# Kernel optimization log

Hardware: AMD Instinct MI355X
Metric: run time of the kernel (lower is better)

Reference implementation:

```python
import jax, jax.numpy as jnp
import numpy as np

EPS = 1e-5  # torch BatchNorm2d default eps


def _conv(x, w, pad=0, groups=1):
    # x: NCHW, w: OIHW (torch layout); matches nn.Conv2d with given padding/groups
    return jax.lax.conv_general_dilated(
        x, w, window_strides=(1, 1), padding=[(pad, pad), (pad, pad)],
        dimension_numbers=("NCHW", "OIHW", "NCHW"), feature_group_count=groups)


def _bn_train(x, gamma, beta):
    # BatchNorm2d in training mode: batch stats over (N,H,W), biased variance
    m = jnp.mean(x, axis=(0, 2, 3), keepdims=True)
    v = jnp.mean(jnp.square(x - m), axis=(0, 2, 3), keepdims=True)
    return (x - m) * jax.lax.rsqrt(v + EPS) * gamma.reshape(1, -1, 1, 1) + beta.reshape(1, -1, 1, 1)


def setup_inputs() -> dict:
    key = jax.random.key(0)
    ks = jax.random.split(key, 8)
    B, C, H, W = 8, 32, 128, 128
    D = 8                      # num_directions
    WC = C * D                 # wavelet_channels = 256
    MID = WC * 2               # 512
    x = jax.random.normal(ks[0], (B, C, H, W), jnp.float32)
    # grouped directional filter bank: Conv2d(C, C*D, k=5, groups=C, bias=False)
    w_dir = jax.random.normal(ks[1], (WC, 1, 5, 5), jnp.float32) / np.sqrt(25.0)
    # wavelet_conv: Conv(WC->MID,3) BN ReLU Conv(MID->WC,3) BN ReLU
    w1 = jax.random.normal(ks[2], (MID, WC, 3, 3), jnp.float32) / np.sqrt(WC * 9.0)
    b1 = jnp.zeros((MID,), jnp.float32)
    g1 = jnp.ones((MID,), jnp.float32)
    be1 = jnp.zeros((MID,), jnp.float32)
    w2 = jax.random.normal(ks[3], (WC, MID, 3, 3), jnp.float32) / np.sqrt(MID * 9.0)
    b2 = jnp.zeros((WC,), jnp.float32)
    g2 = jnp.ones((WC,), jnp.float32)
    be2 = jnp.zeros((WC,), jnp.float32)
    # inverse_conv: Conv2d(WC, C, 1)
    w_inv = jax.random.normal(ks[4], (C, WC, 1, 1), jnp.float32) / np.sqrt(float(WC))
    b_inv = jnp.zeros((C,), jnp.float32)
    return {"x": x, "w_dir": w_dir, "w1": w1, "b1": b1, "g1": g1, "be1": be1,
            "w2": w2, "b2": b2, "g2": g2, "be2": be2, "w_inv": w_inv, "b_inv": b_inv}


def reference(x, w_dir, w1, b1, g1, be1, w2, b2, g2, be2, w_inv, b_inv):
    C = x.shape[1]
    # directional wavelet: grouped conv C -> C*8, k=5, pad=2, no bias
    coeffs = _conv(x, w_dir, pad=2, groups=C)                      # (B, 8C, H, W)
    # wavelet-domain conv stack
    h = _conv(coeffs, w1, pad=1) + b1.reshape(1, -1, 1, 1)         # (B, 16C, H, W)
    h = jax.nn.relu(_bn_train(h, g1, be1))
    h = _conv(h, w2, pad=1) + b2.reshape(1, -1, 1, 1)              # (B, 8C, H, W)
    h = jax.nn.relu(_bn_train(h, g2, be2))
    # inverse 1x1 conv back to C channels
    return _conv(h, w_inv) + b_inv.reshape(1, -1, 1, 1)            # (B, C, H, W)
```

## Files before the change

### kernel.cpp

```cpp
#include <hip/hip_runtime.h>

typedef unsigned short u16;
typedef unsigned int   u32;
typedef __attribute__((ext_vector_type(8)))  __bf16 bf16x8;
typedef __attribute__((ext_vector_type(4)))  float  f32x4;
typedef __attribute__((ext_vector_type(16))) float  f32x16;

__device__ __forceinline__ float bf2f(u16 u) {
    union { u32 i; float f; } v; v.i = ((u32)u) << 16; return v.f;
}
__device__ __forceinline__ u16 f2bf(float f) {
    u32 u = __float_as_uint(f);
    u32 r = (u + 0x7FFFu + ((u >> 16) & 1u)) >> 16;
    return (u16)r;
}

__device__ __forceinline__ void gl16(const u16* g, u16* l) {
    __builtin_amdgcn_global_load_lds(
        (const __attribute__((address_space(1))) unsigned int*)g,
        (__attribute__((address_space(3))) unsigned int*)l, 16, 0, 0);
}

__global__ __launch_bounds__(256) void dir_conv_k(const float* __restrict__ x,
                                                  const float* __restrict__ wd,
                                                  u16* __restrict__ coeffs) {
    int bid = blockIdx.x;
    int cc = bid & 3, y = (bid >> 2) & 127, n = bid >> 9;
    __shared__ float lx[5280];
    __shared__ float lw[1600];
    int t = threadIdx.x;
    for (int i = t; i < 1600; i += 256) {
        int ol = i / 25, tap = i - ol * 25;
        lw[tap * 64 + ol] = wd[(cc * 64 + ol) * 25 + tap];
    }
    for (int i = t; i < 5280; i += 256) {
        int c = i / 660, rem = i - c * 660;
        int ky = rem / 132, xx = rem - ky * 132;
        int gy = y - 2 + ky, gx = xx - 2;
        float v = 0.f;
        if (gy >= 0 && gy < 128 && gx >= 0 && gx < 128)
            v = x[(((n * 32 + cc * 8 + c) * 128 + gy) << 7) + gx];
        lx[i] = v;
    }
    __syncthreads();
    int px = t >> 1, oh = t & 1;
    float acc[4][8];
#pragma unroll
    for (int j = 0; j < 4; ++j)
#pragma unroll
        for (int d = 0; d < 8; ++d) acc[j][d] = 0.f;
#pragma unroll
    for (int j = 0; j < 4; ++j) {
        int cl = oh * 4 + j;
        const float* lxc = &lx[cl * 660];
#pragma unroll
        for (int ky = 0; ky < 5; ++ky)
#pragma unroll
            for (int kx = 0; kx < 5; ++kx) {
                float xv = lxc[ky * 132 + px + kx];
                const float* w8 = &lw[(ky * 5 + kx) * 64 + cl * 8];
#pragma unroll
                for (int d = 0; d < 8; ++d) acc[j][d] += xv * w8[d];
            }
    }
    long base = ((long)((n * 128 + y) * 128 + px)) * 256 + cc * 64 + oh * 32;
#pragma unroll
    for (int j = 0; j < 4; ++j) {
        uint4 o;
        o.x = (u32)f2bf(acc[j][0]) | ((u32)f2bf(acc[j][1]) << 16);
        o.y = (u32)f2bf(acc[j][2]) | ((u32)f2bf(acc[j][3]) << 16);
        o.z = (u32)f2bf(acc[j][4]) | ((u32)f2bf(acc[j][5]) << 16);
        o.w = (u32)f2bf(acc[j][6]) | ((u32)f2bf(acc[j][7]) << 16);
        *(uint4*)(coeffs + base + j * 8) = o;
    }
}

__global__ __launch_bounds__(256) void repack_w_k(const float* __restrict__ w,
                                                  u16* __restrict__ wp,
                                                  int OC, int IC, int total) {
    int f = blockIdx.x * 256 + threadIdx.x;
    if (f >= total) return;
    int KC = IC >> 5;
    int j  = f & 7;
    int h  = (f >> 3) & 1;
    int g  = f >> 4;
    int oc = g % OC; g /= OC;
    int s  = g & 1;  g >>= 1;
    int kc = g % KC;
    int tap = g / KC;
    int ic = kc * 32 + s * 16 + h * 8 + j;
    wp[f] = f2bf(w[(oc * IC + ic) * 9 + tap]);
}

template<int IC, int OC>
__global__ __launch_bounds__(256, 2) void conv3_k(const u16* __restrict__ base,
                                                  u32 in_off,
                                                  const u16* __restrict__ wp,
                                                  const float* __restrict__ bias,
                                                  u32 zp_off,
                                                  u16* __restrict__ outp) {
    constexpr int KC = IC / 32;
    constexpr int W  = 130;
    constexpr int TU = 12 * W;
    constexpr int NFULL = TU / 256;
    constexpr int REM   = TU % 256;
    __shared__ u16 lA0[TU * 8];
    __shared__ u16 lA1[TU * 8];

    int bx = blockIdx.x;
    int y = bx & 127, n = bx >> 7;
    int ocb = blockIdx.y;
    int t = threadIdx.x, lane = t & 63, wv = t >> 6;
    int lm = lane & 31, h = lane >> 5;
    int ocw = ocb * 256 + wv * 64;

    u32 off[NFULL + 1];
#pragma unroll
    for (int i = 0; i <= NFULL; ++i) {
        int u = (i == NFULL) ? (NFULL * 256 + lane) : (i * 256 + t);
        int icq = u / (3 * W);
        int r2  = u - icq * (3 * W);
        int dy  = r2 / W;
        int xx  = r2 - dy * W;
        int gy = y - 1 + dy, gx = xx - 1;
        bool ok = ((unsigned)gy < 128u) && ((unsigned)gx < 128u);
        off[i] = ok ? (in_off + (u32)((n * 128 + gy) * 128 + gx) * IC + (icq & 3) * 8)
                    : zp_off;
    }

    auto stage = [&](u16* dst, int kc) {
#pragma unroll
        for (int i = 0; i < NFULL; ++i)
            gl16(base + off[i] + kc * 32, dst + (i * 256 + wv * 64) * 8);
        if (wv == 0 && lane < REM)
            gl16(base + off[NFULL] + kc * 32, dst + NFULL * 256 * 8);
    };

    bf16x8 B[6][2];
    u32 wboff = (u32)(ocw + lm) * 16 + h * 8;
#pragma unroll
    for (int dx = 0; dx < 3; ++dx)
#pragma unroll
        for (int s = 0; s < 2; ++s) {
            u32 wo = wboff + (u32)((dx * KC) * 2 + s) * (OC * 16);
            B[dx * 2 + s][0] = *(const bf16x8*)(wp + wo);
            B[dx * 2 + s][1] = *(const bf16x8*)(wp + wo + 512);
        }

    f32x16 acc[4][2];
#pragma unroll
    for (int mf = 0; mf < 4; ++mf)
#pragma unroll
        for (int nf = 0; nf < 2; ++nf)
#pragma unroll
            for (int r = 0; r < 16; ++r) acc[mf][nf][r] = 0.f;

    auto compDy = [&](const u16* lAu, int dyU, int dyN, int kcN) {
#pragma unroll
        for (int dx = 0; dx < 3; ++dx)
#pragma unroll
            for (int s = 0; s < 2; ++s) {
                int i = dx * 2 + s;
                int au = (((s * 2 + h) * 3 + dyU) * W + dx + lm) * 8;
                bf16x8 a0 = *(const bf16x8*)(lAu + au);
                bf16x8 a1 = *(const bf16x8*)(lAu + au + 256);
                bf16x8 a2 = *(const bf16x8*)(lAu + au + 512);
                bf16x8 a3 = *(const bf16x8*)(lAu + au + 768);
                __builtin_amdgcn_s_setprio(1);
                acc[0][0] = __builtin_amdgcn_mfma_f32_32x32x16_bf16(a0, B[i][0], acc[0][0], 0, 0, 0);
                acc[0][1] = __builtin_amdgcn_mfma_f32_32x32x16_bf16(a0, B[i][1], acc[0][1], 0, 0, 0);
                acc[1][0] = __builtin_amdgcn_mfma_f32_32x32x16_bf16(a1, B[i][0], acc[1][0], 0, 0, 0);
                acc[1][1] = __builtin_amdgcn_mfma_f32_32x32x16_bf16(a1, B[i][1], acc[1][1], 0, 0, 0);
                acc[2][0] = __builtin_amdgcn_mfma_f32_32x32x16_bf16(a2, B[i][0], acc[2][0], 0, 0, 0);
                acc[2][1] = __builtin_amdgcn_mfma_f32_32x32x16_bf16(a2, B[i][1], acc[2][1], 0, 0, 0);
                acc[3][0] = __builtin_amdgcn_mfma_f32_32x32x16_bf16(a3, B[i][0], acc[3][0], 0, 0, 0);
                acc[3][1] = __builtin_amdgcn_mfma_f32_32x32x16_bf16(a3, B[i][1], acc[3][1], 0, 0, 0);
                __builtin_amdgcn_s_setprio(0);
                u32 wo = wboff + (u32)(((dyN * 3 + dx) * KC + kcN) * 2 + s) * (OC * 16);
                B[i][0] = *(const bf16x8*)(wp + wo);
                B[i][1] = *(const bf16x8*)(wp + wo + 512);
            }
    };

    stage(lA0, 0);
    for (int kc = 0; kc < KC; kc += 2) {
        __syncthreads();
        stage(lA1, kc + 1);
        compDy(lA0, 0, 1, kc);
        compDy(lA0, 1, 2, kc);
        compDy(lA0, 2, 0, kc + 1);
        __syncthreads();
        if (kc + 2 < KC) stage(lA0, kc + 2);
        compDy(lA1, 0, 1, kc + 1);
        compDy(lA1, 1, 2, kc + 1);
        compDy(lA1, 2, 0, (kc + 2 < KC) ? kc + 2 : 0);
    }

    long rowb = (long)(n * 128 + y) * 128;
#pragma unroll
    for (int mf = 0; mf < 4; ++mf)
#pragma unroll
        for (int nf = 0; nf < 2; ++nf) {
            int oc = ocw + nf * 32 + lm;
            float bi = bias[oc];
#pragma unroll
            for (int r = 0; r < 16; ++r) {
                int px = mf * 32 + (r & 3) + ((r >> 2) << 3) + (h << 2);
                outp[(rowb + px) * OC + oc] = f2bf(acc[mf][nf][r] + bi);
            }
        }
}

template<int C>
__global__ __launch_bounds__(256) void stats1_k(const u16* __restrict__ h,
                                                float* __restrict__ part) {
    constexpr int CH2 = C / 2;
    constexpr int PARTS = 256 / CH2;
    constexpr int RPB = 1024;
    constexpr int RPT = RPB / PARTS;
    int t = threadIdx.x;
    int chp = t % CH2, rp = t / CH2;
    long row0 = (long)blockIdx.x * RPB + (long)rp * RPT;
    float s0 = 0.f, q0 = 0.f, s1 = 0.f, q1 = 0.f;
    const u16* base = h + row0 * C + chp * 2;
    for (int r = 0; r < RPT; ++r) {
        u32 v = *(const u32*)(base + (long)r * C);
        float a = bf2f((u16)(v & 0xffff));
        float b = bf2f((u16)(v >> 16));
        s0 += a; q0 += a * a; s1 += b; q1 += b * b;
    }
    float4 o = make_float4(s0, q0, s1, q1);
    *(float4*)(part + ((long)(blockIdx.x * PARTS + rp) * CH2 + chp) * 4) = o;
}

template<int C>
__global__ __launch_bounds__(256) void stats2_k(const float* __restrict__ part,
                                                const float* __restrict__ g,
                                                const float* __restrict__ be,
                                                float* __restrict__ ab) {
    constexpr int CH2 = C / 2;
    constexpr int NP = 128 * (256 / CH2);
    int ch = blockIdx.x * 256 + threadIdx.x;
    if (ch >= C) return;
    int chp = ch >> 1, lo = ch & 1;
    float s = 0.f, q = 0.f;
    for (int p = 0; p < NP; ++p) {
        s += part[((long)p * CH2 + chp) * 4 + lo * 2];
        q += part[((long)p * CH2 + chp) * 4 + lo * 2 + 1];
    }
    const float M = 131072.f;
    float mean = s / M;
    float var = q / M - mean * mean;
    float a = g[ch] * rsqrtf(var + 1e-5f);
    ab[ch * 2]     = a;
    ab[ch * 2 + 1] = be[ch] - mean * a;
}

__global__ __launch_bounds__(256) void bn_relu_k(u16* __restrict__ h,
                                                 const float* __restrict__ ab) {
    long idx8 = (long)blockIdx.x * 256 + threadIdx.x;
    u16* p = h + idx8 * 8;
    uint4 v = *(const uint4*)p;
    int chb = ((int)idx8 & 63) << 3;
    u32 w[4] = {v.x, v.y, v.z, v.w};
    u32 o[4];
#pragma unroll
    for (int q = 0; q < 4; ++q) {
        int ch = chb + q * 2;
        float2 a0 = *(const float2*)(ab + ch * 2);
        float2 a1 = *(const float2*)(ab + ch * 2 + 2);
        float f0 = bf2f((u16)(w[q] & 0xffff));
        float f1 = bf2f((u16)(w[q] >> 16));
        f0 = fmaxf(f0 * a0.x + a0.y, 0.f);
        f1 = fmaxf(f1 * a1.x + a1.y, 0.f);
        o[q] = (u32)f2bf(f0) | ((u32)f2bf(f1) << 16);
    }
    *(uint4*)p = make_uint4(o[0], o[1], o[2], o[3]);
}

__global__ __launch_bounds__(256) void inv_conv_k(const u16* __restrict__ h2,
                                                  const float* __restrict__ ab,
                                                  const float* __restrict__ winv,
                                                  const float* __restrict__ binv,
                                                  float* __restrict__ out) {
    __shared__ float lw[8192];
    __shared__ float lab[512];
    int t = threadIdx.x;
    for (int i = t; i < 8192; i += 256) {
        int k = i >> 5, oc = i & 31;
        lw[i] = winv[oc * 256 + k];
    }
    lab[t] = ab[t];
    lab[t + 256] = ab[t + 256];
    __syncthreads();
    long p = (long)blockIdx.x * 256 + t;
    const u16* hp = h2 + p * 256;
    f32x4 acc[8];
    f32x4 zero = {0.f, 0.f, 0.f, 0.f};
#pragma unroll
    for (int q = 0; q < 8; ++q) acc[q] = zero;
    for (int k = 0; k < 256; k += 8) {
        uint4 hv = *(const uint4*)(hp + k);
        u32 wv[4] = {hv.x, hv.y, hv.z, hv.w};
#pragma unroll
        for (int e = 0; e < 8; ++e) {
            u16 us = (e & 1) ? (u16)(wv[e >> 1] >> 16) : (u16)(wv[e >> 1] & 0xffff);
            int kk = k + e;
            float v = bf2f(us);
            v = fmaxf(v * lab[kk * 2] + lab[kk * 2 + 1], 0.f);
            const f32x4* w4 = (const f32x4*)(lw + kk * 32);
#pragma unroll
            for (int q = 0; q < 8; ++q) acc[q] += v * w4[q];
        }
    }
    int n = (int)(p >> 14), rem = (int)(p & 16383);
#pragma unroll
    for (int q = 0; q < 8; ++q)
#pragma unroll
        for (int c = 0; c < 4; ++c) {
            int oc = q * 4 + c;
            out[((long)(n * 32 + oc) << 14) + rem] = acc[q][c] + binv[oc];
        }
}

extern "C" void kernel_launch(void* const* d_in, const int* in_sizes, int n_in,
                              void* d_out, int out_size, void* d_ws, size_t ws_size,
                              hipStream_t stream) {
    const float* x     = (const float*)d_in[0];
    const float* w_dir = (const float*)d_in[1];
    const float* w1    = (const float*)d_in[2];
    const float* b1    = (const float*)d_in[3];
    const float* g1    = (const float*)d_in[4];
    const float* be1   = (const float*)d_in[5];
    const float* w2    = (const float*)d_in[6];
    const float* b2    = (const float*)d_in[7];
    const float* g2    = (const float*)d_in[8];
    const float* be2   = (const float*)d_in[9];
    const float* w_inv = (const float*)d_in[10];
    const float* b_inv = (const float*)d_in[11];
    float* out = (float*)d_out;
    char* ws = (char*)d_ws;

    u16*   w1p  = (u16*)(ws + 0);
    u16*   w2p  = (u16*)(ws + 2359296);
    float* part = (float*)(ws + 4718592);
    float* ab1  = (float*)(ws + 5242880);
    float* ab2  = (float*)(ws + 5246976);
    u16*   zp   = (u16*)(ws + 5249024);
    u16*   coef = (u16*)(ws + 8388608);
    u16*   h1   = (u16*)(ws + 75497472);
    const u16* basep = (const u16*)ws;
    u32 zp_off   = 5249024 / 2;
    u32 coef_off = 8388608 / 2;
    u32 h1_off   = 75497472 / 2;

    hipMemsetAsync(zp, 0, 1024, stream);
    repack_w_k<<<4608, 256, 0, stream>>>(w1, w1p, 512, 256, 1179648);
    repack_w_k<<<4608, 256, 0, stream>>>(w2, w2p, 256, 512, 1179648);
    dir_conv_k<<<4096, 256, 0, stream>>>(x, w_dir, coef);
    conv3_k<256, 512><<<dim3(1024, 2), 256, 0, stream>>>(basep, coef_off, w1p, b1, zp_off, h1);
    stats1_k<512><<<128, 256, 0, stream>>>(h1, part);
    stats2_k<512><<<2, 256, 0, stream>>>(part, g1, be1, ab1);
    bn_relu_k<<<32768, 256, 0, stream>>>(h1, ab1);
    conv3_k<512, 256><<<dim3(1024, 1), 256, 0, stream>>>(basep, h1_off, w2p, b2, zp_off, coef);
    stats1_k<256><<<128, 256, 0, stream>>>(coef, part);
    stats2_k<256><<<1, 256, 0, stream>>>(part, g2, be2, ab2);
    inv_conv_k<<<512, 256, 0, stream>>>(coef, ab2, w_inv, b_inv, out);
}
```

Measured before the change: 821.1 us.

## Fuse BN statistics into conv epilogue and software-pipeline conv inner loop

Batch-norm sum and sum-of-squares are now accumulated in the conv3 epilogue and added to a per-channel buffer with atomics, which removes the separate stats1 pass that re-read the large bf16 activations. stats2 now only reads the final sums. The conv inner loop is restructured into a single per-kc loop with double-buffered A/B register prefetch, and the block index is remapped to interleave batches. Atomics add contention and make the summation order nondeterministic; the single-pass variance formula in fp32 stays.

Measured after the change: 729.7 us. 11.1% less time.

```diff
diff --git a/kernel.cpp b/kernel.cpp
--- a/kernel.cpp
+++ b/kernel.cpp
@@ -98,7 +98,8 @@
                                                   const u16* __restrict__ wp,
                                                   const float* __restrict__ bias,
                                                   u32 zp_off,
-                                                  u16* __restrict__ outp) {
+                                                  u16* __restrict__ outp,
+                                                  float* __restrict__ statp) {
     constexpr int KC = IC / 32;
     constexpr int W  = 130;
     constexpr int TU = 12 * W;
@@ -107,7 +108,8 @@
     __shared__ u16 lA0[TU * 8];
     __shared__ u16 lA1[TU * 8];
 
-    int bx = blockIdx.x;
+    int bx0 = blockIdx.x;
+    int bx = ((bx0 & 7) << 7) + (bx0 >> 3);
     int y = bx & 127, n = bx >> 7;
     int ocb = blockIdx.y;
     int t = threadIdx.x, lane = t & 63, wv = t >> 6;
@@ -136,16 +138,15 @@
             gl16(base + off[NFULL] + kc * 32, dst + NFULL * 256 * 8);
     };
 
-    bf16x8 B[6][2];
     u32 wboff = (u32)(ocw + lm) * 16 + h * 8;
-#pragma unroll
-    for (int dx = 0; dx < 3; ++dx)
-#pragma unroll
-        for (int s = 0; s < 2; ++s) {
-            u32 wo = wboff + (u32)((dx * KC) * 2 + s) * (OC * 16);
-            B[dx * 2 + s][0] = *(const bf16x8*)(wp + wo);
-            B[dx * 2 + s][1] = *(const bf16x8*)(wp + wo + 512);
-        }
+    bf16x8 Ar[2][4];
+    bf16x8 Br[2][2];
+
+    {
+        const u16* wb = wp + wboff;
+        Br[0][0] = *(const bf16x8*)wb;
+        Br[0][1] = *(const bf16x8*)(wb + 512);
+    }
 
     f32x16 acc[4][2];
 #pragma unroll
@@ -155,82 +156,81 @@
 #pragma unroll
             for (int r = 0; r < 16; ++r) acc[mf][nf][r] = 0.f;
 
-    auto compDy = [&](const u16* lAu, int dyU, int dyN, int kcN) {
-#pragma unroll
-        for (int dx = 0; dx < 3; ++dx)
-#pragma unroll
-            for (int s = 0; s < 2; ++s) {
-                int i = dx * 2 + s;
-                int au = (((s * 2 + h) * 3 + dyU) * W + dx + lm) * 8;
-                bf16x8 a0 = *(const bf16x8*)(lAu + au);
-                bf16x8 a1 = *(const bf16x8*)(lAu + au + 256);
-                bf16x8 a2 = *(const bf16x8*)(lAu + au + 512);
-                bf16x8 a3 = *(const bf16x8*)(lAu + au + 768);
-                __builtin_amdgcn_s_setprio(1);
-                acc[0][0] = __builtin_amdgcn_mfma_f32_32x32x16_bf16(a0, B[i][0], acc[0][0], 0, 0, 0);
-                acc[0][1] = __builtin_amdgcn_mfma_f32_32x32x16_bf16(a0, B[i][1], acc[0][1], 0, 0, 0);
-                acc[1][0] = __builtin_amdgcn_mfma_f32_32x32x16_bf16(a1, B[i][0], acc[1][0], 0, 0, 0);
-                acc[1][1] = __builtin_amdgcn_mfma_f32_32x32x16_bf16(a1, B[i][1], acc[1][1], 0, 0, 0);
-                acc[2][0] = __builtin_amdgcn_mfma_f32_32x32x16_bf16(a2, B[i][0], acc[2][0], 0, 0, 0);
-                acc[2][1] = __builtin_amdgcn_mfma_f32_32x32x16_bf16(a2, B[i][1], acc[2][1], 0, 0, 0);
-                acc[3][0] = __builtin_amdgcn_mfma_f32_32x32x16_bf16(a3, B[i][0], acc[3][0], 0, 0, 0);
-                acc[3][1] = __builtin_amdgcn_mfma_f32_32x32x16_bf16(a3, B[i][1], acc[3][1], 0, 0, 0);
-                __builtin_amdgcn_s_setprio(0);
-                u32 wo = wboff + (u32)(((dyN * 3 + dx) * KC + kcN) * 2 + s) * (OC * 16);
-                B[i][0] = *(const bf16x8*)(wp + wo);
-                B[i][1] = *(const bf16x8*)(wp + wo + 512);
+    stage(lA0, 0);
+    for (int kc = 0; kc < KC; ++kc) {
+        const u16* lAu = (kc & 1) ? lA1 : lA0;
+        u16*       lAn = (kc & 1) ? lA0 : lA1;
+        __syncthreads();
+        {
+            int au = ((h * 3) * W + lm) * 8;
+            Ar[0][0] = *(const bf16x8*)(lAu + au);
+            Ar[0][1] = *(const bf16x8*)(lAu + au + 256);
+            Ar[0][2] = *(const bf16x8*)(lAu + au + 512);
+            Ar[0][3] = *(const bf16x8*)(lAu + au + 768);
+        }
+        if (kc + 1 < KC) stage(lAn, kc + 1);
+#pragma unroll
+        for (int i = 0; i < 18; ++i) {
+            const int j   = (i + 1) % 18;
+            const int jdy = j / 6, jdx = (j % 6) >> 1, js = j & 1;
+            const int jkc = (i == 17) ? ((kc + 1 < KC) ? kc + 1 : 0) : kc;
+            if (i != 17) {
+                int au = (((js * 2 + h) * 3 + jdy) * W + jdx + lm) * 8;
+                Ar[j & 1][0] = *(const bf16x8*)(lAu + au);
+                Ar[j & 1][1] = *(const bf16x8*)(lAu + au + 256);
+                Ar[j & 1][2] = *(const bf16x8*)(lAu + au + 512);
+                Ar[j & 1][3] = *(const bf16x8*)(lAu + au + 768);
             }
-    };
-
-    stage(lA0, 0);
-    for (int kc = 0; kc < KC; kc += 2) {
-        __syncthreads();
-        stage(lA1, kc + 1);
-        compDy(lA0, 0, 1, kc);
-        compDy(lA0, 1, 2, kc);
-        compDy(lA0, 2, 0, kc + 1);
-        __syncthreads();
-        if (kc + 2 < KC) stage(lA0, kc + 2);
-        compDy(lA1, 0, 1, kc + 1);
-        compDy(lA1, 1, 2, kc + 1);
-        compDy(lA1, 2, 0, (kc + 2 < KC) ? kc + 2 : 0);
+            {
+                const u16* wb = wp + wboff
+                    + (u32)(((jdy * 3 + jdx) * KC + jkc) * 2 + js) * (OC * 16);
+                Br[j & 1][0] = *(const bf16x8*)wb;
+                Br[j & 1][1] = *(const bf16x8*)(wb + 512);
+            }
+            __builtin_amdgcn_s_setprio(1);
+            acc[0][0] = __builtin_amdgcn_mfma_f32_32x32x16_bf16(Ar[i & 1][0], Br[i & 1][0], acc[0][0], 0, 0, 0);
+            acc[0][1] = __builtin_amdgcn_mfma_f32_32x32x16_bf16(Ar[i & 1][0], Br[i & 1][1], acc[0][1], 0, 0, 0);
+            acc[1][0] = __builtin_amdgcn_mfma_f32_32x32x16_bf16(Ar[i & 1][1], Br[i & 1][0], acc[1][0], 0, 0, 0);
+            acc[1][1] = __builtin_amdgcn_mfma_f32_32x32x16_bf16(Ar[i & 1][1], Br[i & 1][1], acc[1][1], 0, 0, 0);
+            acc[2][0] = __builtin_amdgcn_mfma_f32_32x32x16_bf16(Ar[i & 1][2], Br[i & 1][0], acc[2][0], 0, 0, 0);
+            acc[2][1] = __builtin_amdgcn_mfma_f32_32x32x16_bf16(Ar[i & 1][2], Br[i & 1][1], acc[2][1], 0, 0, 0);
+            acc[3][0] = __builtin_amdgcn_mfma_f32_32x32x16_bf16(Ar[i & 1][3], Br[i & 1][0], acc[3][0], 0, 0, 0);
+            acc[3][1] = __builtin_amdgcn_mfma_f32_32x32x16_bf16(Ar[i & 1][3], Br[i & 1][1], acc[3][1], 0, 0, 0);
+            __builtin_amdgcn_s_setprio(0);
+        }
     }
 
     long rowb = (long)(n * 128 + y) * 128;
-#pragma unroll
-    for (int mf = 0; mf < 4; ++mf)
+    float ss[2] = {0.f, 0.f}, qq[2] = {0.f, 0.f};
+#pragma unroll
+    for (int nf = 0; nf < 2; ++nf) {
+        int oc = ocw + nf * 32 + lm;
+        float bi = bias[oc];
+#pragma unroll
+        for (int mf = 0; mf < 4; ++mf)
+#pragma unroll
+            for (int r = 0; r < 16; ++r) {
+                int px = mf * 32 + (r & 3) + ((r >> 2) << 3) + (h << 2);
+                u16 bv = f2bf(acc[mf][nf][r] + bi);
+                outp[(rowb + px) * OC + oc] = bv;
+                float vr = bf2f(bv);
+                ss[nf] += vr;
+                qq[nf] += vr * vr;
+            }
+    }
+#pragma unroll
+    for (int nf = 0; nf < 2; ++nf) {
+        ss[nf] += __shfl_xor(ss[nf], 32);
+        qq[nf] += __shfl_xor(qq[nf], 32);
+    }
+    if (h == 0) {
 #pragma unroll
         for (int nf = 0; nf < 2; ++nf) {
             int oc = ocw + nf * 32 + lm;
-            float bi = bias[oc];
-#pragma unroll
-            for (int r = 0; r < 16; ++r) {
-                int px = mf * 32 + (r & 3) + ((r >> 2) << 3) + (h << 2);
-                outp[(rowb + px) * OC + oc] = f2bf(acc[mf][nf][r] + bi);
-            }
-        }
-}
-
-template<int C>
-__global__ __launch_bounds__(256) void stats1_k(const u16* __restrict__ h,
-                                                float* __restrict__ part) {
-    constexpr int CH2 = C / 2;
-    constexpr int PARTS = 256 / CH2;
-    constexpr int RPB = 1024;
-    constexpr int RPT = RPB / PARTS;
-    int t = threadIdx.x;
-    int chp = t % CH2, rp = t / CH2;
-    long row0 = (long)blockIdx.x * RPB + (long)rp * RPT;
-    float s0 = 0.f, q0 = 0.f, s1 = 0.f, q1 = 0.f;
-    const u16* base = h + row0 * C + chp * 2;
-    for (int r = 0; r < RPT; ++r) {
-        u32 v = *(const u32*)(base + (long)r * C);
-        float a = bf2f((u16)(v & 0xffff));
-        float b = bf2f((u16)(v >> 16));
-        s0 += a; q0 += a * a; s1 += b; q1 += b * b;
-    }
-    float4 o = make_float4(s0, q0, s1, q1);
-    *(float4*)(part + ((long)(blockIdx.x * PARTS + rp) * CH2 + chp) * 4) = o;
+            atomicAdd(&statp[oc * 2],     ss[nf]);
+            atomicAdd(&statp[oc * 2 + 1], qq[nf]);
+        }
+    }
 }
 
 template<int C>
@@ -238,16 +238,9 @@
                                                 const float* __restrict__ g,
                                                 const float* __restrict__ be,
                                                 float* __restrict__ ab) {
-    constexpr int CH2 = C / 2;
-    constexpr int NP = 128 * (256 / CH2);
     int ch = blockIdx.x * 256 + threadIdx.x;
     if (ch >= C) return;
-    int chp = ch >> 1, lo = ch & 1;
-    float s = 0.f, q = 0.f;
-    for (int p = 0; p < NP; ++p) {
-        s += part[((long)p * CH2 + chp) * 4 + lo * 2];
-        q += part[((long)p * CH2 + chp) * 4 + lo * 2 + 1];
-    }
+    float s = part[ch * 2], q = part[ch * 2 + 1];
     const float M = 131072.f;
     float mean = s / M;
     float var = q / M - mean * mean;
@@ -341,29 +334,29 @@
     float* out = (float*)d_out;
     char* ws = (char*)d_ws;
 
-    u16*   w1p  = (u16*)(ws + 0);
-    u16*   w2p  = (u16*)(ws + 2359296);
-    float* part = (float*)(ws + 4718592);
-    float* ab1  = (float*)(ws + 5242880);
-    float* ab2  = (float*)(ws + 5246976);
-    u16*   zp   = (u16*)(ws + 5249024);
-    u16*   coef = (u16*)(ws + 8388608);
-    u16*   h1   = (u16*)(ws + 75497472);
+    u16*   w1p   = (u16*)(ws + 0);
+    u16*   w2p   = (u16*)(ws + 2359296);
+    float* part1 = (float*)(ws + 4718592);
+    float* part2 = (float*)(ws + 4722688);
+    float* ab1   = (float*)(ws + 5242880);
+    float* ab2   = (float*)(ws + 5246976);
+    u16*   zp    = (u16*)(ws + 5249024);
+    u16*   coef  = (u16*)(ws + 8388608);
+    u16*   h1    = (u16*)(ws + 75497472);
     const u16* basep = (const u16*)ws;
     u32 zp_off   = 5249024 / 2;
     u32 coef_off = 8388608 / 2;
     u32 h1_off   = 75497472 / 2;
 
     hipMemsetAsync(zp, 0, 1024, stream);
+    hipMemsetAsync(part1, 0, 8192, stream);
     repack_w_k<<<4608, 256, 0, stream>>>(w1, w1p, 512, 256, 1179648);
     repack_w_k<<<4608, 256, 0, stream>>>(w2, w2p, 256, 512, 1179648);
     dir_conv_k<<<4096, 256, 0, stream>>>(x, w_dir, coef);
-    conv3_k<256, 512><<<dim3(1024, 2), 256, 0, stream>>>(basep, coef_off, w1p, b1, zp_off, h1);
-    stats1_k<512><<<128, 256, 0, stream>>>(h1, part);
-    stats2_k<512><<<2, 256, 0, stream>>>(part, g1, be1, ab1);
+    conv3_k<256, 512><<<dim3(1024, 2), 256, 0, stream>>>(basep, coef_off, w1p, b1, zp_off, h1, part1);
+    stats2_k<512><<<2, 256, 0, stream>>>(part1, g1, be1, ab1);
     bn_relu_k<<<32768, 256, 0, stream>>>(h1, ab1);
-    conv3_k<512, 256><<<dim3(1024, 1), 256, 0, stream>>>(basep, h1_off, w2p, b2, zp_off, coef);
-    stats1_k<256><<<128, 256, 0, stream>>>(coef, part);
-    stats2_k<256><<<1, 256, 0, stream>>>(part, g2, be2, ab2);
+    conv3_k<512, 256><<<dim3(1024, 1), 256, 0, stream>>>(basep, h1_off, w2p, b2, zp_off, coef, part2);
+    stats2_k<256><<<1, 256, 0, stream>>>(part2, g2, be2, ab2);
     inv_conv_k<<<512, 256, 0, stream>>>(coef, ab2, w_inv, b_inv, out);
 }
```
